# Kernel tuning notes

Measured on AMD Instinct MI355X. Metric: run time of the kernel, lower is better.

Reference implementation:

```python
import jax, jax.numpy as jnp
import numpy as np

HUMAN_CONF = 0.7
KP_CONF = 0.5
NMS_THR = 0.5


def _cxcywh_to_xyxy(b):
    cx, cy, w, h = b[..., 0], b[..., 1], b[..., 2], b[..., 3]
    return jnp.stack([cx - 0.5 * w, cy - 0.5 * h, cx + 0.5 * w, cy + 0.5 * h], axis=-1)


def _iou_matrix(boxes):  # [Q,4] xyxy -> [Q,Q]
    area = jnp.maximum(boxes[:, 2] - boxes[:, 0], 0) * jnp.maximum(boxes[:, 3] - boxes[:, 1], 0)
    lt = jnp.maximum(boxes[:, None, :2], boxes[None, :, :2])
    rb = jnp.minimum(boxes[:, None, 2:], boxes[None, :, 2:])
    wh = jnp.maximum(rb - lt, 0)
    inter = wh[..., 0] * wh[..., 1]
    union = area[:, None] + area[None, :] - inter
    return inter / jnp.maximum(union, 1e-9)


def _nms(boxes, scores, valid, thr):
    # Greedy NMS over score-sorted boxes; invalid boxes never kept.
    Q = scores.shape[0]
    order = jnp.argsort(jnp.where(valid, scores, -jnp.inf))[::-1]
    b, v = boxes[order], valid[order]
    iou = _iou_matrix(b)
    idxs = jnp.arange(Q)

    def body(sup, i):
        keep_i = v[i] & jnp.logical_not(sup[i])
        sup = sup | (keep_i & (iou[i] > thr) & (idxs != i))
        return sup, keep_i

    _, keeps = jax.lax.scan(body, jnp.zeros(Q, bool), idxs)
    return jnp.zeros(Q, bool).at[order].set(keeps)


def _roi_kps(hm, box, sx, sy):
    # hm: [K,H,W] float, box: [4] int32 (xyxy in image coords).
    # Masked full-map argmax == ROI-crop argmax of the original (outside = -inf).
    K, H, W = hm.shape
    x1 = jnp.maximum((box[0].astype(jnp.float32) * sx).astype(jnp.int32), 0)
    y1 = jnp.maximum((box[1].astype(jnp.float32) * sy).astype(jnp.int32), 0)
    x2 = jnp.minimum((box[2].astype(jnp.float32) * sx).astype(jnp.int32) + 1, W)
    y2 = jnp.minimum((box[3].astype(jnp.float32) * sy).astype(jnp.int32) + 1, H)
    xs, ys = jnp.arange(W), jnp.arange(H)
    mask = ((ys >= y1) & (ys < y2))[:, None] & ((xs >= x1) & (xs < x2))[None, :]
    flat = jnp.where(mask[None], hm, -jnp.inf).reshape(K, -1)
    max_vals = flat.max(-1)
    idx = flat.argmax(-1)
    col = (idx % W).astype(jnp.float32)
    row = (idx // W).astype(jnp.float32)
    kps = jnp.stack([col / sx, row / sy, max_vals], -1)  # [K,3]
    ok = (x2 > x1) & (y2 > y1)
    return jnp.where(ok, kps, 0.0)


def setup_inputs() -> dict:
    key = jax.random.key(0)
    k1, k2, k3 = jax.random.split(key, 3)
    B, Q, K, Hh, Wh = 4, 100, 17, 128, 128
    return {
        "human_logits": jax.random.normal(k1, (B, Q, 2), jnp.float32) * 2.0,
        "pred_boxes": jax.random.uniform(k2, (B, Q, 4), jnp.float32),
        "pred_heatmaps": jax.random.normal(k3, (B, K, Hh, Wh), jnp.float32),
        "img_h": 512,
        "img_w": 512,
    }


def reference(human_logits, pred_boxes, pred_heatmaps, img_h, img_w):
    K, Hh, Wh = pred_heatmaps.shape[1:]
    prob = jax.nn.softmax(human_logits, -1)
    scores = prob.max(-1)          # [B,Q]
    labels = prob.argmax(-1)       # [B,Q]
    scale = jnp.array([img_w, img_h, img_w, img_h], jnp.float32)
    boxes = _cxcywh_to_xyxy(pred_boxes) * scale  # [B,Q,4] image coords
    valid = (labels == 0) & (scores >= HUMAN_CONF)
    keep = jax.vmap(lambda b, s, v: _nms(b, s, v, NMS_THR))(boxes, scores, valid)  # [B,Q] bool
    boxes_int = boxes.astype(jnp.int32)
    sx, sy = Wh / img_w, Hh / img_h
    kps = jax.vmap(lambda hm, bx: jax.vmap(lambda b: _roi_kps(hm, b, sx, sy))(bx))(
        pred_heatmaps, boxes_int)  # [B,Q,K,3]
    conf = kps[..., 2]
    kps = kps.at[..., 2].set(jnp.where(conf < KP_CONF, 0.0, conf))
    keep_f = keep.astype(jnp.float32)
    scores_out = scores * keep_f
    kps_out = kps * keep_f[:, :, None, None]
    boxes_out = boxes_int * keep[:, :, None]
    return scores_out, boxes_out, kps_out, keep
```

## Files before the change

### kernel.cpp

```cpp
#include <hip/hip_runtime.h>
#include <cmath>
#include <cfloat>

constexpr int NB = 4;
constexpr int NQ = 100;
constexpr int NK = 17;
constexpr int NH = 128;
constexpr int NW = 128;

constexpr float HUMAN_CONF = 0.7f;
constexpr float KP_CONF    = 0.5f;
constexpr float NMS_THR    = 0.5f;

constexpr int OFF_BOXES = NB * NQ;
constexpr int OFF_KPS   = NB * NQ * 5;
constexpr int OFF_KEEP  = NB * NQ * 5 + NB * NQ * NK * 3;

__global__ __launch_bounds__(128) void score_nms_kernel(
    const float* __restrict__ logits,
    const float* __restrict__ pboxes,
    const int* __restrict__ img_h_p,
    const int* __restrict__ img_w_p,
    float* __restrict__ out,
    int* __restrict__ wcount,
    int2* __restrict__ wlist)
{
    const int b = blockIdx.x;
    const int t = threadIdx.x;

    __shared__ float sbx[NQ][4];
    __shared__ float ssc[NQ];
    __shared__ unsigned char sval[NQ];
    __shared__ int   sorder[NQ];
    __shared__ float sortb[NQ][4];
    __shared__ float sarea[NQ];
    __shared__ unsigned char ssv[NQ];
    __shared__ unsigned long long smask0[NQ], smask1[NQ];
    __shared__ unsigned long long skmask[2];
    __shared__ unsigned long long swl0;

    {
        float* kz = out + OFF_KPS + b * (NQ * NK * 3);
        for (int i = t; i < NQ * NK * 3; i += 128) kz[i] = 0.0f;
    }

    const float iw = (float)img_w_p[0];
    const float ih = (float)img_h_p[0];
    const float sx = (float)NW / iw;
    const float sy = (float)NH / ih;

    if (t < NQ) {
        const float l0 = logits[(b * NQ + t) * 2 + 0];
        const float l1 = logits[(b * NQ + t) * 2 + 1];
        const float m  = fmaxf(l0, l1);
        const float e0 = expf(l0 - m);
        const float e1 = expf(l1 - m);
        const float score = fmaxf(e0, e1) / (e0 + e1);
        const bool  lab0  = (l0 >= l1);

        const float cx = pboxes[(b * NQ + t) * 4 + 0];
        const float cy = pboxes[(b * NQ + t) * 4 + 1];
        const float w  = pboxes[(b * NQ + t) * 4 + 2];
        const float h  = pboxes[(b * NQ + t) * 4 + 3];
        sbx[t][0] = (cx - 0.5f * w) * iw;
        sbx[t][1] = (cy - 0.5f * h) * ih;
        sbx[t][2] = (cx + 0.5f * w) * iw;
        sbx[t][3] = (cy + 0.5f * h) * ih;
        ssc[t]  = score;
        sval[t] = (lab0 && score >= HUMAN_CONF) ? 1 : 0;
    }
    __syncthreads();

    if (t < NQ) {
        const float key = sval[t] ? ssc[t] : -INFINITY;
        int rank = 0;
        for (int j = 0; j < NQ; ++j) {
            const float kj = sval[j] ? ssc[j] : -INFINITY;
            if (kj > key || (kj == key && j > t)) rank++;
        }
        sorder[rank] = t;
    }
    __syncthreads();

    if (t < NQ) {
        const int oi = sorder[t];
        const float x1 = sbx[oi][0], y1 = sbx[oi][1], x2 = sbx[oi][2], y2 = sbx[oi][3];
        sortb[t][0] = x1; sortb[t][1] = y1; sortb[t][2] = x2; sortb[t][3] = y2;
        sarea[t] = fmaxf(x2 - x1, 0.0f) * fmaxf(y2 - y1, 0.0f);
        ssv[t]   = sval[oi];
    }
    __syncthreads();

    if (t < NQ) {
        unsigned long long m0 = 0ull, m1 = 0ull;
        const float ax1 = sortb[t][0], ay1 = sortb[t][1], ax2 = sortb[t][2], ay2 = sortb[t][3];
        const float aa = sarea[t];
        for (int j = 0; j < NQ; ++j) {
            const float lx = fmaxf(ax1, sortb[j][0]);
            const float ly = fmaxf(ay1, sortb[j][1]);
            const float rx = fminf(ax2, sortb[j][2]);
            const float ry = fminf(ay2, sortb[j][3]);
            const float wv = fmaxf(rx - lx, 0.0f);
            const float hv = fmaxf(ry - ly, 0.0f);
            const float inter = wv * hv;
            const float uni = aa + sarea[j] - inter;
            const float iou = inter / fmaxf(uni, 1e-9f);
            if (iou > NMS_THR) {
                if (j < 64) m0 |= 1ull << j; else m1 |= 1ull << (j - 64);
            }
        }
        smask0[t] = m0; smask1[t] = m1;
    }
    __syncthreads();

    if (t == 0) {
        unsigned long long sup0 = 0ull, sup1 = 0ull, k0 = 0ull, k1 = 0ull;
        for (int i = 0; i < NQ; ++i) {
            if (!ssv[i]) break;
            const bool sup = (i < 64) ? ((sup0 >> i) & 1ull) : ((sup1 >> (i - 64)) & 1ull);
            if (!sup) {
                if (i < 64) k0 |= 1ull << i; else k1 |= 1ull << (i - 64);
                sup0 |= smask0[i];
                sup1 |= smask1[i];
            }
        }
        skmask[0] = k0; skmask[1] = k1;
    }
    __syncthreads();

    int  kp = 0, gi = 0;
    int  x1i = 0, y1i = 0, x2i = 0, y2i = 0;
    bool live = false;

    if (t < NQ) {
        const int oi = sorder[t];
        kp = (t < 64) ? (int)((skmask[0] >> t) & 1ull)
                      : (int)((skmask[1] >> (t - 64)) & 1ull);
        gi = b * NQ + oi;

        out[gi] = ssc[oi] * (float)kp;

        const int bi0 = (int)sbx[oi][0];
        const int bi1 = (int)sbx[oi][1];
        const int bi2 = (int)sbx[oi][2];
        const int bi3 = (int)sbx[oi][3];
        out[OFF_BOXES + gi * 4 + 0] = (float)(bi0 * kp);
        out[OFF_BOXES + gi * 4 + 1] = (float)(bi1 * kp);
        out[OFF_BOXES + gi * 4 + 2] = (float)(bi2 * kp);
        out[OFF_BOXES + gi * 4 + 3] = (float)(bi3 * kp);

        out[OFF_KEEP + gi] = (float)kp;

        x1i = max((int)((float)bi0 * sx), 0);
        y1i = max((int)((float)bi1 * sy), 0);
        x2i = min((int)((float)bi2 * sx) + 1, NW);
        y2i = min((int)((float)bi3 * sy) + 1, NH);
        live = kp && (x2i > x1i) && (y2i > y1i);
    }

    const unsigned long long lm = __ballot(live);
    if (t == 0) swl0 = lm;
    __syncthreads();
    if (t == 64) wcount[b] = __popcll(swl0) + __popcll(lm);
    const int lane = t & 63;
    const unsigned long long below = lm & ((lane ? (1ull << lane) : 1ull) - 1ull);
    const int rank = (t < 64) ? __popcll(below) : __popcll(swl0) + __popcll(below);
    if (live) {
        const int pack = x1i | (y1i << 8) | (x2i << 16) | (y2i << 24);
        wlist[b * NQ + rank] = make_int2(pack, gi);
    }
}

__global__ __launch_bounds__(64) void kps_kernel(
    const float* __restrict__ hm,
    const int* __restrict__ wcount,
    const int2* __restrict__ wlist,
    const int* __restrict__ img_h_p,
    const int* __restrict__ img_w_p,
    float* __restrict__ out)
{
    const int bb  = blockIdx.x;
    const int b   = bb / (NQ * NK);
    const int rem = bb - b * (NQ * NK);
    const int r   = rem / NK;
    const int k   = rem - r * NK;

    if (r >= wcount[b]) return;

    const int2 wl = wlist[b * NQ + r];
    const int x1 = wl.x & 255;
    const int y1 = (wl.x >> 8) & 255;
    const int x2 = (wl.x >> 16) & 255;
    const int y2 = (wl.x >> 24) & 255;
    const int gi = wl.y;

    const int lane = threadIdx.x;
    const float sx = (float)NW / (float)img_w_p[0];
    const float sy = (float)NH / (float)img_h_p[0];

    const float4* __restrict__ b4 =
        (const float4*)(hm + (size_t)(b * NK + k) * (NH * NW));

    const int xa     = x1 & ~3;
    const int C4     = (x2 - xa + 3) >> 2;
    const int R      = y2 - y1;
    const int total4 = R * C4;
    const unsigned M = (C4 > 1) ? (0xFFFFFFFFu / (unsigned)C4 + 1u) : 0u;

    float best = -INFINITY;
    int   bidx = 0x7fffffff;

    auto proc = [&](int idx, float4 v) {
        const int row = (C4 == 1) ? idx : (int)__umulhi((unsigned)idx, M);
        const int xb  = xa + (idx - row * C4) * 4;
        const int g   = (y1 + row) * NW + xb;
        const float v0 = (xb + 0 >= x1 && xb + 0 < x2) ? v.x : -INFINITY;
        const float v1 = (xb + 1 >= x1 && xb + 1 < x2) ? v.y : -INFINITY;
        const float v2 = (xb + 2 >= x1 && xb + 2 < x2) ? v.z : -INFINITY;
        const float v3 = (xb + 3 < x2) ? v.w : -INFINITY;
        if (v0 > best) { best = v0; bidx = g + 0; }
        if (v1 > best) { best = v1; bidx = g + 1; }
        if (v2 > best) { best = v2; bidx = g + 2; }
        if (v3 > best) { best = v3; bidx = g + 3; }
    };
    auto caddr = [&](int idx) {
        const int row = (C4 == 1) ? idx : (int)__umulhi((unsigned)idx, M);
        return (y1 + row) * (NW / 4) + (xa >> 2) + (idx - row * C4);
    };

    int idx = lane;
    for (; idx + 192 < total4; idx += 256) {
        const int a0 = caddr(idx), a1 = caddr(idx + 64), a2 = caddr(idx + 128), a3 = caddr(idx + 192);
        const float4 v0 = b4[a0];
        const float4 v1 = b4[a1];
        const float4 v2 = b4[a2];
        const float4 v3 = b4[a3];
        proc(idx, v0);
        proc(idx + 64, v1);
        proc(idx + 128, v2);
        proc(idx + 192, v3);
    }
    for (; idx < total4; idx += 64) proc(idx, b4[caddr(idx)]);

    for (int off = 32; off >= 1; off >>= 1) {
        const float ov = __shfl_down(best, off);
        const int   oi = __shfl_down(bidx, off);
        if (ov > best || (ov == best && oi < bidx)) { best = ov; bidx = oi; }
    }

    if (lane == 0) {
        const int col = bidx & (NW - 1);
        const int row = bidx >> 7;
        float conf = best;
        if (conf < KP_CONF) conf = 0.0f;
        float* kout = out + OFF_KPS + (size_t)gi * (NK * 3) + k * 3;
        kout[0] = (float)col / sx;
        kout[1] = (float)row / sy;
        kout[2] = conf;
    }
}

extern "C" void kernel_launch(void* const* d_in, const int* in_sizes, int n_in,
                              void* d_out, int out_size, void* d_ws, size_t ws_size,
                              hipStream_t stream) {
    const float* logits = (const float*)d_in[0];
    const float* pboxes = (const float*)d_in[1];
    const float* hm     = (const float*)d_in[2];
    const int*   img_h  = (const int*)d_in[3];
    const int*   img_w  = (const int*)d_in[4];
    float* out = (float*)d_out;

    int*  wcount = (int*)d_ws;
    int2* wlist  = (int2*)((char*)d_ws + 256);

    score_nms_kernel<<<NB, 128, 0, stream>>>(logits, pboxes, img_h, img_w, out, wcount, wlist);
    kps_kernel<<<NB * NQ * NK, 64, 0, stream>>>(hm, wcount, wlist, img_h, img_w, out);
}
```

Before: 108.1 us.

## Compact keypoint work into a grid-stride persistent loop and use ballot-based NMS

The keypoint kernel now launches a fixed grid of 2048 blocks that grid-stride over a compacted list of live (batch, box, keypoint) items, computed from per-batch counts, instead of launching 6800 blocks where most exit early. The greedy NMS loop is rewritten to visit only remaining valid candidates, using a ballot-built validity mask and count-trailing-zeros. The zero-fill of the keypoint output is widened to float4 stores. The aim is to cut block launch and scheduling overhead for empty work and to shorten the serial NMS loop. The cost is an extra per-item decode inside the loop and possible load imbalance when few items are live.

```diff
diff --git a/kernel.cpp b/kernel.cpp
--- a/kernel.cpp
+++ b/kernel.cpp
@@ -37,11 +37,13 @@
     __shared__ unsigned char ssv[NQ];
     __shared__ unsigned long long smask0[NQ], smask1[NQ];
     __shared__ unsigned long long skmask[2];
+    __shared__ unsigned long long svb[2];
     __shared__ unsigned long long swl0;
 
     {
-        float* kz = out + OFF_KPS + b * (NQ * NK * 3);
-        for (int i = t; i < NQ * NK * 3; i += 128) kz[i] = 0.0f;
+        float4* kz4 = (float4*)(out + OFF_KPS + b * (NQ * NK * 3));
+        const float4 z4 = make_float4(0.0f, 0.0f, 0.0f, 0.0f);
+        for (int i = t; i < (NQ * NK * 3) / 4; i += 128) kz4[i] = z4;
     }
 
     const float iw = (float)img_w_p[0];
@@ -111,18 +113,25 @@
         }
         smask0[t] = m0; smask1[t] = m1;
     }
+
+    {
+        const bool sv = (t < NQ) ? (ssv[t] != 0) : false;
+        const unsigned long long vb = __ballot(sv);
+        if ((t & 63) == 0) svb[t >> 6] = vb;
+    }
     __syncthreads();
 
     if (t == 0) {
-        unsigned long long sup0 = 0ull, sup1 = 0ull, k0 = 0ull, k1 = 0ull;
-        for (int i = 0; i < NQ; ++i) {
-            if (!ssv[i]) break;
-            const bool sup = (i < 64) ? ((sup0 >> i) & 1ull) : ((sup1 >> (i - 64)) & 1ull);
-            if (!sup) {
-                if (i < 64) k0 |= 1ull << i; else k1 |= 1ull << (i - 64);
-                sup0 |= smask0[i];
-                sup1 |= smask1[i];
-            }
+        unsigned long long rem0 = svb[0], rem1 = svb[1];
+        unsigned long long k0 = 0ull, k1 = 0ull;
+        while (rem0 | rem1) {
+            int i;
+            unsigned long long bit0 = 0ull, bit1 = 0ull;
+            if (rem0) { i = __builtin_ctzll(rem0); bit0 = 1ull << i; }
+            else      { const int j = __builtin_ctzll(rem1); i = 64 + j; bit1 = 1ull << j; }
+            k0 |= bit0; k1 |= bit1;
+            rem0 &= ~(smask0[i] | bit0);
+            rem1 &= ~(smask1[i] | bit1);
         }
         skmask[0] = k0; skmask[1] = k1;
     }
@@ -179,84 +188,91 @@
     const int* __restrict__ img_w_p,
     float* __restrict__ out)
 {
-    const int bb  = blockIdx.x;
-    const int b   = bb / (NQ * NK);
-    const int rem = bb - b * (NQ * NK);
-    const int r   = rem / NK;
-    const int k   = rem - r * NK;
-
-    if (r >= wcount[b]) return;
-
-    const int2 wl = wlist[b * NQ + r];
-    const int x1 = wl.x & 255;
-    const int y1 = (wl.x >> 8) & 255;
-    const int x2 = (wl.x >> 16) & 255;
-    const int y2 = (wl.x >> 24) & 255;
-    const int gi = wl.y;
+    const int c0 = wcount[0] * NK;
+    const int c1 = wcount[1] * NK;
+    const int c2 = wcount[2] * NK;
+    const int c3 = wcount[3] * NK;
+    const int t0 = c0, t1 = c0 + c1, t2 = t1 + c2, T = t2 + c3;
 
     const int lane = threadIdx.x;
     const float sx = (float)NW / (float)img_w_p[0];
     const float sy = (float)NH / (float)img_h_p[0];
 
-    const float4* __restrict__ b4 =
-        (const float4*)(hm + (size_t)(b * NK + k) * (NH * NW));
-
-    const int xa     = x1 & ~3;
-    const int C4     = (x2 - xa + 3) >> 2;
-    const int R      = y2 - y1;
-    const int total4 = R * C4;
-    const unsigned M = (C4 > 1) ? (0xFFFFFFFFu / (unsigned)C4 + 1u) : 0u;
-
-    float best = -INFINITY;
-    int   bidx = 0x7fffffff;
-
-    auto proc = [&](int idx, float4 v) {
-        const int row = (C4 == 1) ? idx : (int)__umulhi((unsigned)idx, M);
-        const int xb  = xa + (idx - row * C4) * 4;
-        const int g   = (y1 + row) * NW + xb;
-        const float v0 = (xb + 0 >= x1 && xb + 0 < x2) ? v.x : -INFINITY;
-        const float v1 = (xb + 1 >= x1 && xb + 1 < x2) ? v.y : -INFINITY;
-        const float v2 = (xb + 2 >= x1 && xb + 2 < x2) ? v.z : -INFINITY;
-        const float v3 = (xb + 3 < x2) ? v.w : -INFINITY;
-        if (v0 > best) { best = v0; bidx = g + 0; }
-        if (v1 > best) { best = v1; bidx = g + 1; }
-        if (v2 > best) { best = v2; bidx = g + 2; }
-        if (v3 > best) { best = v3; bidx = g + 3; }
-    };
-    auto caddr = [&](int idx) {
-        const int row = (C4 == 1) ? idx : (int)__umulhi((unsigned)idx, M);
-        return (y1 + row) * (NW / 4) + (xa >> 2) + (idx - row * C4);
-    };
-
-    int idx = lane;
-    for (; idx + 192 < total4; idx += 256) {
-        const int a0 = caddr(idx), a1 = caddr(idx + 64), a2 = caddr(idx + 128), a3 = caddr(idx + 192);
-        const float4 v0 = b4[a0];
-        const float4 v1 = b4[a1];
-        const float4 v2 = b4[a2];
-        const float4 v3 = b4[a3];
-        proc(idx, v0);
-        proc(idx + 64, v1);
-        proc(idx + 128, v2);
-        proc(idx + 192, v3);
-    }
-    for (; idx < total4; idx += 64) proc(idx, b4[caddr(idx)]);
-
-    for (int off = 32; off >= 1; off >>= 1) {
-        const float ov = __shfl_down(best, off);
-        const int   oi = __shfl_down(bidx, off);
-        if (ov > best || (ov == best && oi < bidx)) { best = ov; bidx = oi; }
-    }
-
-    if (lane == 0) {
-        const int col = bidx & (NW - 1);
-        const int row = bidx >> 7;
-        float conf = best;
-        if (conf < KP_CONF) conf = 0.0f;
-        float* kout = out + OFF_KPS + (size_t)gi * (NK * 3) + k * 3;
-        kout[0] = (float)col / sx;
-        kout[1] = (float)row / sy;
-        kout[2] = conf;
+    for (int item = blockIdx.x; item < T; item += gridDim.x) {
+        int b, base;
+        if (item < t1) { if (item < t0) { b = 0; base = 0;  } else { b = 1; base = t0; } }
+        else           { if (item < t2) { b = 2; base = t1; } else { b = 3; base = t2; } }
+        const int local = item - base;
+        const int r = local / NK;
+        const int k = local - r * NK;
+
+        const int2 wl = wlist[b * NQ + r];
+        const int x1 = wl.x & 255;
+        const int y1 = (wl.x >> 8) & 255;
+        const int x2 = (wl.x >> 16) & 255;
+        const int y2 = (wl.x >> 24) & 255;
+        const int gi = wl.y;
+
+        const float4* __restrict__ b4 =
+            (const float4*)(hm + (size_t)(b * NK + k) * (NH * NW));
+
+        const int xa     = x1 & ~3;
+        const int C4     = (x2 - xa + 3) >> 2;
+        const int R      = y2 - y1;
+        const int total4 = R * C4;
+        const unsigned M = (C4 > 1) ? (0xFFFFFFFFu / (unsigned)C4 + 1u) : 0u;
+
+        float best = -INFINITY;
+        int   bidx = 0x7fffffff;
+
+        auto proc = [&](int idx, float4 v) {
+            const int row = (C4 == 1) ? idx : (int)__umulhi((unsigned)idx, M);
+            const int xb  = xa + (idx - row * C4) * 4;
+            const int g   = (y1 + row) * NW + xb;
+            const float v0 = (xb + 0 >= x1 && xb + 0 < x2) ? v.x : -INFINITY;
+            const float v1 = (xb + 1 >= x1 && xb + 1 < x2) ? v.y : -INFINITY;
+            const float v2 = (xb + 2 >= x1 && xb + 2 < x2) ? v.z : -INFINITY;
+            const float v3 = (xb + 3 < x2) ? v.w : -INFINITY;
+            if (v0 > best) { best = v0; bidx = g + 0; }
+            if (v1 > best) { best = v1; bidx = g + 1; }
+            if (v2 > best) { best = v2; bidx = g + 2; }
+            if (v3 > best) { best = v3; bidx = g + 3; }
+        };
+        auto caddr = [&](int idx) {
+            const int row = (C4 == 1) ? idx : (int)__umulhi((unsigned)idx, M);
+            return (y1 + row) * (NW / 4) + (xa >> 2) + (idx - row * C4);
+        };
+
+        int idx = lane;
+        for (; idx + 192 < total4; idx += 256) {
+            const int a0 = caddr(idx), a1 = caddr(idx + 64), a2 = caddr(idx + 128), a3 = caddr(idx + 192);
+            const float4 v0 = b4[a0];
+            const float4 v1 = b4[a1];
+            const float4 v2 = b4[a2];
+            const float4 v3 = b4[a3];
+            proc(idx, v0);
+            proc(idx + 64, v1);
+            proc(idx + 128, v2);
+            proc(idx + 192, v3);
+        }
+        for (; idx < total4; idx += 64) proc(idx, b4[caddr(idx)]);
+
+        for (int off = 32; off >= 1; off >>= 1) {
+            const float ov = __shfl_down(best, off);
+            const int   oi = __shfl_down(bidx, off);
+            if (ov > best || (ov == best && oi < bidx)) { best = ov; bidx = oi; }
+        }
+
+        if (lane == 0) {
+            const int col = bidx & (NW - 1);
+            const int row = bidx >> 7;
+            float conf = best;
+            if (conf < KP_CONF) conf = 0.0f;
+            float* kout = out + OFF_KPS + (size_t)gi * (NK * 3) + k * 3;
+            kout[0] = (float)col / sx;
+            kout[1] = (float)row / sy;
+            kout[2] = conf;
+        }
     }
 }
 
@@ -274,5 +290,5 @@
     int2* wlist  = (int2*)((char*)d_ws + 256);
 
     score_nms_kernel<<<NB, 128, 0, stream>>>(logits, pboxes, img_h, img_w, out, wcount, wlist);
-    kps_kernel<<<NB * NQ * NK, 64, 0, stream>>>(hm, wcount, wlist, img_h, img_w, out);
+    kps_kernel<<<2048, 64, 0, stream>>>(hm, wcount, wlist, img_h, img_w, out);
 }
```

Result: no change. 106.6 us (-1.3%).
